# Performance work log

Hardware: AMD Instinct MI355X
Metric: run time of the kernel (lower is better)

Reference implementation:

```python
import jax, jax.numpy as jnp
import numpy as np

N = 50000      # nodes per node type (shared: same edge_index reused across types)
E = 500000     # edges per edge type
H, C = 4, 32   # GATConv heads=4, out_channels = 128 // 4
HID = 128
NEG_SLOPE = 0.2  # PyG GATConv leaky_relu default


def gat(x, src, dst, W, att_src, att_dst, bias):
    """PyG GATConv (eval mode: dropout off), default add_self_loops=True, concat heads."""
    n = x.shape[0]
    xp = (x @ W).reshape(n, H, C)                       # [n, H, C]
    s_src = jnp.einsum('nhc,hc->nh', xp, att_src)       # per-node src scores
    s_dst = jnp.einsum('nhc,hc->nh', xp, att_dst)       # per-node dst scores
    loop = jnp.arange(n, dtype=src.dtype)
    s = jnp.concatenate([src, loop])                    # self-loops appended
    d = jnp.concatenate([dst, loop])
    e = jax.nn.leaky_relu(s_src[s] + s_dst[d], NEG_SLOPE)   # [E+n, H]
    m = jax.ops.segment_max(e, d, num_segments=n)       # segment softmax over incoming edges
    ex = jnp.exp(e - m[d])
    denom = jax.ops.segment_sum(ex, d, num_segments=n)
    alpha = ex / denom[d]                               # [E+n, H]
    out = jax.ops.segment_sum(alpha[:, :, None] * xp[s], d, num_segments=n)  # [n, H, C]
    return out.reshape(n, H * C) + bias


def setup_inputs() -> dict:
    key = jax.random.key(0)
    ks = jax.random.split(key, 24)
    def lin(k, din, dout):
        return (jax.random.normal(k, (din, dout), jnp.float32) / np.sqrt(din)).astype(jnp.float32)
    inp = {}
    inp['x_account'] = jax.random.normal(ks[0], (N, 64), jnp.float32)
    inp['x_customer'] = jax.random.normal(ks[1], (N, 32), jnp.float32)
    inp['x_transaction'] = jax.random.normal(ks[2], (N, 128), jnp.float32)
    inp['ei_transacts'] = jax.random.randint(ks[3], (2, E), 0, N, dtype=jnp.int32)
    inp['ei_owns'] = jax.random.randint(ks[4], (2, E), 0, N, dtype=jnp.int32)
    inp['ei_shares'] = jax.random.randint(ks[5], (2, E), 0, N, dtype=jnp.int32)
    # node embedding Linears
    inp['W_acc'] = lin(ks[6], 64, HID);  inp['b_acc'] = jnp.zeros((HID,), jnp.float32)
    inp['W_cus'] = lin(ks[7], 32, HID);  inp['b_cus'] = jnp.zeros((HID,), jnp.float32)
    inp['W_txn'] = lin(ks[8], 128, HID); inp['b_txn'] = jnp.zeros((HID,), jnp.float32)
    # GATConv params for the two LIVE edge types (first edge type's GATConv is dead code)
    inp['Wg_owns'] = lin(ks[9], HID, H * C)
    inp['as_owns'] = jax.random.normal(ks[10], (H, C), jnp.float32) * 0.1
    inp['ad_owns'] = jax.random.normal(ks[11], (H, C), jnp.float32) * 0.1
    inp['bg_owns'] = jnp.zeros((H * C,), jnp.float32)
    inp['Wg_shares'] = lin(ks[12], HID, H * C)
    inp['as_shares'] = jax.random.normal(ks[13], (H, C), jnp.float32) * 0.1
    inp['ad_shares'] = jax.random.normal(ks[14], (H, C), jnp.float32) * 0.1
    inp['bg_shares'] = jnp.zeros((H * C,), jnp.float32)
    # classifier
    inp['W_cls'] = lin(ks[15], HID, 1); inp['b_cls'] = jnp.zeros((1,), jnp.float32)
    return inp


def reference(x_account, x_customer, x_transaction,
              ei_transacts, ei_owns, ei_shares,
              W_acc, b_acc, W_cus, b_cus, W_txn, b_txn,
              Wg_owns, as_owns, ad_owns, bg_owns,
              Wg_shares, as_shares, ad_shares, bg_shares,
              W_cls, b_cls):
    # per-type embedding (dict insertion order: account, customer, transaction)
    emb = [x_account @ W_acc + b_acc,
           x_customer @ W_cus + b_cus,
           x_transaction @ W_txn + b_txn]
    # edge type 1 ('transacts') initializes final embeddings; types 2,3 add GAT outputs
    finals = []
    for h in emb:
        f = h
        f = f + gat(h, ei_owns[0], ei_owns[1], Wg_owns, as_owns, ad_owns, bg_owns)
        f = f + gat(h, ei_shares[0], ei_shares[1], Wg_shares, as_shares, ad_shares, bg_shares)
        finals.append(f)
    combined = jnp.concatenate(finals, axis=0)          # [3N, HID]
    return jax.nn.sigmoid(combined @ W_cls + b_cls)     # [3N, 1]
```

## Files before the change

kernel.cpp:

```cpp
#include <hip/hip_runtime.h>
#include <hip/hip_bf16.h>
#include <math.h>

#define NNODES 50000
#define NEDGES 500000
#define NTILES 1563

__device__ __forceinline__ float lrelu(float x) { return x > 0.f ? x : 0.2f * x; }

__device__ __forceinline__ unsigned short f2bf(float f) {
    unsigned int u = __float_as_uint(f);
    u += 0x7FFFu + ((u >> 16) & 1u);
    return (unsigned short)(u >> 16);
}

__global__ void wprep_kernel(const float* __restrict__ Wt0, const float* __restrict__ Wt1,
                             const float* __restrict__ Wt2,
                             const float* __restrict__ bt0, const float* __restrict__ bt1,
                             const float* __restrict__ bt2,
                             const float* __restrict__ WgO, const float* __restrict__ WgS,
                             const float* __restrict__ Wc,
                             float* __restrict__ Wcomb, float* __restrict__ wc1,
                             float* __restrict__ bcomb, float* __restrict__ c0) {
    __shared__ float wrow[128];
    const int b = blockIdx.x;
    const int t = threadIdx.x;
    const float* src;
    int isBias = 0, ty = 0, k = 0;
    if (b < 64)       { src = Wt0; k = b;       ty = 0; }
    else if (b < 96)  { src = Wt1; k = b - 64;  ty = 1; }
    else if (b < 224) { src = Wt2; k = b - 96;  ty = 2; }
    else              { isBias = 1; ty = b - 224; src = (ty == 0) ? bt0 : (ty == 1) ? bt1 : bt2; }
    if (t < 128) wrow[t] = isBias ? src[t] : src[k * 128 + t];
    __syncthreads();
    const float* Wg = (t < 128) ? WgO : WgS;
    const int j = t & 127;
    float acc = 0.f;
#pragma unroll 8
    for (int m = 0; m < 128; m++) acc += wrow[m] * Wg[m * 128 + j];
    if (isBias) bcomb[ty * 256 + t] = acc;
    else        Wcomb[b * 256 + t] = acc;
    if (t < 64) {
        float s = wrow[t] * Wc[t] + wrow[t + 64] * Wc[t + 64];
#pragma unroll
        for (int o = 32; o > 0; o >>= 1) s += __shfl_xor(s, o);
        if (t == 0) { if (isBias) c0[ty] = s; else wc1[b] = s; }
    }
}

__launch_bounds__(256)
__global__ void xp_all_b(const float* __restrict__ X0, const float* __restrict__ X1,
                         const float* __restrict__ X2,
                         const float* __restrict__ Wcomb, const float* __restrict__ wc1,
                         const float* __restrict__ bcomb, const float* __restrict__ c0,
                         const float* __restrict__ asO, const float* __restrict__ adO,
                         const float* __restrict__ asS, const float* __restrict__ adS,
                         float* __restrict__ embPart,
                         unsigned short* __restrict__ xpO, unsigned short* __restrict__ xpS,
                         float* __restrict__ ssO, float* __restrict__ sdO,
                         float* __restrict__ ssS, float* __restrict__ sdS, int n) {
    __shared__ float xs[32][128];
    const int t = threadIdx.x;
    const int j4 = t & 31, r = t >> 5;
    const int tile = blockIdx.x % NTILES;
    const int type = blockIdx.x / NTILES;
    const int row0 = tile * 32;

    const float* X;
    int K, ksh, off;
    if (type == 0)      { X = X0; K = 64;  ksh = 4; off = 0;  }
    else if (type == 1) { X = X1; K = 32;  ksh = 3; off = 64; }
    else                { X = X2; K = 128; ksh = 5; off = 96; }
    const size_t tb = (size_t)type * n;

    const int KQ = K >> 2;
    for (int f = t; f < 32 * KQ; f += 256) {
        int row = f >> ksh, kq = f & (KQ - 1);
        float4 v = {0.f, 0.f, 0.f, 0.f};
        if (row0 + row < n) v = *(const float4*)&X[(size_t)(row0 + row) * K + kq * 4];
        *(float4*)&xs[row][kq * 4] = v;
    }
    __syncthreads();

    float4 aO[4], aS[4];
    float dp[4] = {0.f, 0.f, 0.f, 0.f};
#pragma unroll
    for (int p = 0; p < 4; p++) { aO[p] = {0.f, 0.f, 0.f, 0.f}; aS[p] = {0.f, 0.f, 0.f, 0.f}; }
    const float* wb = Wcomb + (size_t)off * 256;
    const float* w1p = wc1 + off;
#pragma unroll 4
    for (int k = 0; k < K; k++) {
        float4 wo = *(const float4*)&wb[k * 256 + j4 * 4];
        float4 ws = *(const float4*)&wb[k * 256 + 128 + j4 * 4];
        float w1 = w1p[k];
        float x0 = xs[r][k], x1 = xs[r + 8][k], x2 = xs[r + 16][k], x3 = xs[r + 24][k];
        aO[0].x += x0 * wo.x; aO[0].y += x0 * wo.y; aO[0].z += x0 * wo.z; aO[0].w += x0 * wo.w;
        aO[1].x += x1 * wo.x; aO[1].y += x1 * wo.y; aO[1].z += x1 * wo.z; aO[1].w += x1 * wo.w;
        aO[2].x += x2 * wo.x; aO[2].y += x2 * wo.y; aO[2].z += x2 * wo.z; aO[2].w += x2 * wo.w;
        aO[3].x += x3 * wo.x; aO[3].y += x3 * wo.y; aO[3].z += x3 * wo.z; aO[3].w += x3 * wo.w;
        aS[0].x += x0 * ws.x; aS[0].y += x0 * ws.y; aS[0].z += x0 * ws.z; aS[0].w += x0 * ws.w;
        aS[1].x += x1 * ws.x; aS[1].y += x1 * ws.y; aS[1].z += x1 * ws.z; aS[1].w += x1 * ws.w;
        aS[2].x += x2 * ws.x; aS[2].y += x2 * ws.y; aS[2].z += x2 * ws.z; aS[2].w += x2 * ws.w;
        aS[3].x += x3 * ws.x; aS[3].y += x3 * ws.y; aS[3].z += x3 * ws.z; aS[3].w += x3 * ws.w;
        dp[0] += x0 * w1; dp[1] += x1 * w1; dp[2] += x2 * w1; dp[3] += x3 * w1;
    }
    float4 bO = *(const float4*)&bcomb[type * 256 + j4 * 4];
    float4 bS = *(const float4*)&bcomb[type * 256 + 128 + j4 * 4];
    const float cc = c0[type];
#pragma unroll
    for (int p = 0; p < 4; p++) {
        aO[p].x += bO.x; aO[p].y += bO.y; aO[p].z += bO.z; aO[p].w += bO.w;
        aS[p].x += bS.x; aS[p].y += bS.y; aS[p].z += bS.z; aS[p].w += bS.w;
    }

    float4 vasO = *(const float4*)&asO[j4 * 4];
    float4 vadO = *(const float4*)&adO[j4 * 4];
    float4 vasS = *(const float4*)&asS[j4 * 4];
    float4 vadS = *(const float4*)&adS[j4 * 4];
#pragma unroll
    for (int p = 0; p < 4; p++) {
        int row = row0 + r + 8 * p;
        if (row < n) {
            ushort4 uo, us;
            uo.x = f2bf(aO[p].x); uo.y = f2bf(aO[p].y); uo.z = f2bf(aO[p].z); uo.w = f2bf(aO[p].w);
            us.x = f2bf(aS[p].x); us.y = f2bf(aS[p].y); us.z = f2bf(aS[p].z); us.w = f2bf(aS[p].w);
            *(ushort4*)&xpO[(tb + row) * 128 + j4 * 4] = uo;
            *(ushort4*)&xpS[(tb + row) * 128 + j4 * 4] = us;
            if (j4 == 0) embPart[tb + row] = dp[p] + cc;
        }
        float psO = aO[p].x * vasO.x + aO[p].y * vasO.y + aO[p].z * vasO.z + aO[p].w * vasO.w;
        float pdO = aO[p].x * vadO.x + aO[p].y * vadO.y + aO[p].z * vadO.z + aO[p].w * vadO.w;
        float psS = aS[p].x * vasS.x + aS[p].y * vasS.y + aS[p].z * vasS.z + aS[p].w * vasS.w;
        float pdS = aS[p].x * vadS.x + aS[p].y * vadS.y + aS[p].z * vadS.z + aS[p].w * vadS.w;
#pragma unroll
        for (int o = 4; o > 0; o >>= 1) {
            psO += __shfl_xor(psO, o);
            pdO += __shfl_xor(pdO, o);
            psS += __shfl_xor(psS, o);
            pdS += __shfl_xor(pdS, o);
        }
        if ((j4 & 7) == 0 && row < n) {
            size_t hidx = (tb + row) * 4 + (j4 >> 3);
            ssO[hidx] = psO; sdO[hidx] = pdO;
            ssS[hidx] = psS; sdS[hidx] = pdS;
        }
    }
}

__global__ void zero_int(int* __restrict__ p, int n) {
    int i = blockIdx.x * blockDim.x + threadIdx.x;
    if (i < n) p[i] = 0;
}

__global__ void count2_kernel(const int* __restrict__ eiO, const int* __restrict__ eiS,
                              int e, int n, int* __restrict__ counts2) {
    int q = blockIdx.x * blockDim.x + threadIdx.x;
    if (q >= 2 * e) return;
    int ty = q >= e;
    int i = ty ? q - e : q;
    const int* ei = ty ? eiS : eiO;
    atomicAdd(&counts2[ty * n + ei[e + i]], 1);
}

__global__ void block_sum_kernel(const int* __restrict__ counts, int n, int* __restrict__ psum) {
    __shared__ int ws[16];
    int tid = threadIdx.x, lane = tid & 63, wid = tid >> 6;
    int i = blockIdx.x * 1024 + tid;
    int v = (i < n) ? counts[i] : 0;
#pragma unroll
    for (int o = 1; o < 64; o <<= 1) v += __shfl_xor(v, o);
    if (lane == 0) ws[wid] = v;
    __syncthreads();
    if (tid < 16) {
        int s = ws[tid];
#pragma unroll
        for (int o = 1; o < 16; o <<= 1) s += __shfl_xor(s, o, 16);
        if (tid == 0) psum[blockIdx.x] = s;
    }
}

__global__ void scan_psum_big(int* __restrict__ psum, int nb, int* __restrict__ total) {
    __shared__ int wsum[2];
    int tid = threadIdx.x, lane = tid & 63, wid = tid >> 6;
    int v = (tid < nb) ? psum[tid] : 0;
    int x = v;
#pragma unroll
    for (int o = 1; o < 64; o <<= 1) {
        int t = __shfl_up(x, o);
        if (lane >= o) x += t;
    }
    if (lane == 63) wsum[wid] = x;
    __syncthreads();
    int base = (wid == 1) ? wsum[0] : 0;
    if (tid < nb) psum[tid] = base + x - v;
    if (tid == 127) *total = wsum[0] + wsum[1];
}

__global__ void scan_block_kernel(const int* __restrict__ counts, const int* __restrict__ psum,
                                  int n, int* __restrict__ row_ptr, int* __restrict__ cursor) {
    __shared__ int ws[16];
    int tid = threadIdx.x, lane = tid & 63, wid = tid >> 6;
    int i = blockIdx.x * 1024 + tid;
    int v = (i < n) ? counts[i] : 0;
    int x = v;
#pragma unroll
    for (int o = 1; o < 64; o <<= 1) {
        int t = __shfl_up(x, o);
        if (lane >= o) x += t;
    }
    if (lane == 63) ws[wid] = x;
    __syncthreads();
    if (tid < 16) {
        int s = ws[tid];
#pragma unroll
        for (int o = 1; o < 16; o <<= 1) {
            int t = __shfl_up(s, o, 16);
            if (tid >= o) s += t;
        }
        ws[tid] = s;
    }
    __syncthreads();
    int base = psum[blockIdx.x] + (wid ? ws[wid - 1] : 0);
    int excl = base + x - v;
    if (i < n) { row_ptr[i] = excl; cursor[i] = excl; }
}

__global__ void scatter2_kernel(const int* __restrict__ eiO, const int* __restrict__ eiS,
                                int e, int n, int* __restrict__ cursor2,
                                long long* __restrict__ cp2) {
    int q = blockIdx.x * blockDim.x + threadIdx.x;
    if (q >= 2 * e) return;
    int ty = q >= e;
    int i = ty ? q - e : q;
    const int* ei = ty ? eiS : eiO;
    int d = ei[e + i];
    int p = atomicAdd(&cursor2[ty * n + d], 1);
    cp2[p] = ((long long)i << 32) | (unsigned)ei[i];
}

__global__ void sort_rows_kernel(const int* __restrict__ rp, long long* __restrict__ cp, int n) {
    int i = blockIdx.x * blockDim.x + threadIdx.x;
    if (i >= n) return;
    int r0 = rp[i], r1 = rp[i + 1];
    for (int a = r0 + 1; a < r1; a++) {
        long long v = cp[a];
        int b = a - 1;
        while (b >= r0 && cp[b] > v) {
            cp[b + 1] = cp[b];
            b--;
        }
        cp[b + 1] = v;
    }
}

__global__ void alpha6_kernel(const int* __restrict__ eiO, const int* __restrict__ eiS,
                              const float* __restrict__ ssO, const float* __restrict__ sdO,
                              const float* __restrict__ ssS, const float* __restrict__ sdS,
                              float* __restrict__ alO, float* __restrict__ alS, int e, int n) {
    int q = blockIdx.x * blockDim.x + threadIdx.x;
    if (q >= 6 * e) return;
    int ty = q / (2 * e);
    int rem = q - ty * 2 * e;
    const size_t nb = (size_t)ty * n * 4;
    const size_t eb = (size_t)ty * e * 4;
    const int* ei;
    const float* ss;
    const float* sd;
    float* al;
    int i;
    if (rem < e) { ei = eiO; ss = ssO + nb; sd = sdO + nb; al = alO + eb; i = rem; }
    else         { ei = eiS; ss = ssS + nb; sd = sdS + nb; al = alS + eb; i = rem - e; }
    int s = ei[i], d = ei[e + i];
    float4 svs = *(const float4*)&ss[s * 4];
    float4 svd = *(const float4*)&ss[d * 4];
    float4 dvd = *(const float4*)&sd[d * 4];
    float4 a;
    a.x = __expf(lrelu(svs.x + dvd.x) - lrelu(svd.x + dvd.x));
    a.y = __expf(lrelu(svs.y + dvd.y) - lrelu(svd.y + dvd.y));
    a.z = __expf(lrelu(svs.z + dvd.z) - lrelu(svd.z + dvd.z));
    a.w = __expf(lrelu(svs.w + dvd.w) - lrelu(svd.w + dvd.w));
    *(float4*)&al[(size_t)i * 4] = a;
}

__global__ void gat_fused_b(const unsigned short* __restrict__ xpO, const float* __restrict__ alO,
                            const unsigned short* __restrict__ xpS, const float* __restrict__ alS,
                            const long long* __restrict__ cp2, const int* __restrict__ rp2,
                            const float* __restrict__ bgO, const float* __restrict__ bgS,
                            const float* __restrict__ embPart, const float* __restrict__ Wc,
                            const float* __restrict__ bc, float* __restrict__ out, int n) {
    const int wave = threadIdx.x >> 6, lane = threadIdx.x & 63;
    const int i3 = blockIdx.x * 4 + wave;
    if (i3 >= 3 * n) return;
    const int ty = i3 / n, i = i3 - ty * n;
    const int c = lane * 2, hh = lane >> 4;

    const unsigned short* xo = xpO + (size_t)ty * n * 128;
    const unsigned short* xs_ = xpS + (size_t)ty * n * 128;
    const float* alo = alO + (size_t)ty * NEDGES * 4;
    const float* als = alS + (size_t)ty * NEDGES * 4;

    const int r0o = rp2[i], r1o = rp2[i + 1];
    const int r0s = rp2[n + i], r1s = rp2[n + i + 1];

    float tO = 0.f, oxO = 0.f, oyO = 0.f;
    float tS = 0.f, oxS = 0.f, oyS = 0.f;
    int ko = r0o, ks = r0s;

    while (ko + 2 <= r1o && ks + 2 <= r1s) {
        long long vo0 = cp2[ko], vo1 = cp2[ko + 1];
        long long vs0 = cp2[ks], vs1 = cp2[ks + 1];
        int so0 = (int)(vo0 & 0xFFFFFFFFll), eo0 = (int)(vo0 >> 32);
        int so1 = (int)(vo1 & 0xFFFFFFFFll), eo1 = (int)(vo1 >> 32);
        int sx0 = (int)(vs0 & 0xFFFFFFFFll), es0 = (int)(vs0 >> 32);
        int sx1 = (int)(vs1 & 0xFFFFFFFFll), es1 = (int)(vs1 >> 32);
        float ao0 = alo[(size_t)eo0 * 4 + hh], ao1 = alo[(size_t)eo1 * 4 + hh];
        float as0 = als[(size_t)es0 * 4 + hh], as1 = als[(size_t)es1 * 4 + hh];
        unsigned uo0 = *(const unsigned*)&xo[(size_t)so0 * 128 + c];
        unsigned uo1 = *(const unsigned*)&xo[(size_t)so1 * 128 + c];
        unsigned us0 = *(const unsigned*)&xs_[(size_t)sx0 * 128 + c];
        unsigned us1 = *(const unsigned*)&xs_[(size_t)sx1 * 128 + c];
        tO += ao0 + ao1;
        oxO += ao0 * __uint_as_float(uo0 << 16) + ao1 * __uint_as_float(uo1 << 16);
        oyO += ao0 * __uint_as_float(uo0 & 0xFFFF0000u) + ao1 * __uint_as_float(uo1 & 0xFFFF0000u);
        tS += as0 + as1;
        oxS += as0 * __uint_as_float(us0 << 16) + as1 * __uint_as_float(us1 << 16);
        oyS += as0 * __uint_as_float(us0 & 0xFFFF0000u) + as1 * __uint_as_float(us1 & 0xFFFF0000u);
        ko += 2; ks += 2;
    }
    while (ko < r1o && ks < r1s) {
        long long vo = cp2[ko], vs = cp2[ks];
        int so = (int)(vo & 0xFFFFFFFFll), eo = (int)(vo >> 32);
        int sx = (int)(vs & 0xFFFFFFFFll), es = (int)(vs >> 32);
        float ao = alo[(size_t)eo * 4 + hh];
        float as_ = als[(size_t)es * 4 + hh];
        unsigned uo = *(const unsigned*)&xo[(size_t)so * 128 + c];
        unsigned us = *(const unsigned*)&xs_[(size_t)sx * 128 + c];
        tO += ao;
        oxO += ao * __uint_as_float(uo << 16);
        oyO += ao * __uint_as_float(uo & 0xFFFF0000u);
        tS += as_;
        oxS += as_ * __uint_as_float(us << 16);
        oyS += as_ * __uint_as_float(us & 0xFFFF0000u);
        ko++; ks++;
    }
    for (; ko + 2 <= r1o; ko += 2) {
        long long vo0 = cp2[ko], vo1 = cp2[ko + 1];
        int so0 = (int)(vo0 & 0xFFFFFFFFll), eo0 = (int)(vo0 >> 32);
        int so1 = (int)(vo1 & 0xFFFFFFFFll), eo1 = (int)(vo1 >> 32);
        float ao0 = alo[(size_t)eo0 * 4 + hh], ao1 = alo[(size_t)eo1 * 4 + hh];
        unsigned uo0 = *(const unsigned*)&xo[(size_t)so0 * 128 + c];
        unsigned uo1 = *(const unsigned*)&xo[(size_t)so1 * 128 + c];
        tO += ao0 + ao1;
        oxO += ao0 * __uint_as_float(uo0 << 16) + ao1 * __uint_as_float(uo1 << 16);
        oyO += ao0 * __uint_as_float(uo0 & 0xFFFF0000u) + ao1 * __uint_as_float(uo1 & 0xFFFF0000u);
    }
    for (; ko < r1o; ko++) {
        long long vo = cp2[ko];
        int so = (int)(vo & 0xFFFFFFFFll), eo = (int)(vo >> 32);
        float ao = alo[(size_t)eo * 4 + hh];
        unsigned uo = *(const unsigned*)&xo[(size_t)so * 128 + c];
        tO += ao;
        oxO += ao * __uint_as_float(uo << 16);
        oyO += ao * __uint_as_float(uo & 0xFFFF0000u);
    }
    for (; ks + 2 <= r1s; ks += 2) {
        long long vs0 = cp2[ks], vs1 = cp2[ks + 1];
        int sx0 = (int)(vs0 & 0xFFFFFFFFll), es0 = (int)(vs0 >> 32);
        int sx1 = (int)(vs1 & 0xFFFFFFFFll), es1 = (int)(vs1 >> 32);
        float as0 = als[(size_t)es0 * 4 + hh], as1 = als[(size_t)es1 * 4 + hh];
        unsigned us0 = *(const unsigned*)&xs_[(size_t)sx0 * 128 + c];
        unsigned us1 = *(const unsigned*)&xs_[(size_t)sx1 * 128 + c];
        tS += as0 + as1;
        oxS += as0 * __uint_as_float(us0 << 16) + as1 * __uint_as_float(us1 << 16);
        oyS += as0 * __uint_as_float(us0 & 0xFFFF0000u) + as1 * __uint_as_float(us1 & 0xFFFF0000u);
    }
    for (; ks < r1s; ks++) {
        long long vs = cp2[ks];
        int sx = (int)(vs & 0xFFFFFFFFll), es = (int)(vs >> 32);
        float as_ = als[(size_t)es * 4 + hh];
        unsigned us = *(const unsigned*)&xs_[(size_t)sx * 128 + c];
        tS += as_;
        oxS += as_ * __uint_as_float(us << 16);
        oyS += as_ * __uint_as_float(us & 0xFFFF0000u);
    }
    {
        unsigned uo = *(const unsigned*)&xo[(size_t)i * 128 + c];
        unsigned us = *(const unsigned*)&xs_[(size_t)i * 128 + c];
        oxO += __uint_as_float(uo << 16);
        oyO += __uint_as_float(uo & 0xFFFF0000u);
        oxS += __uint_as_float(us << 16);
        oyS += __uint_as_float(us & 0xFFFF0000u);
    }
    const float idO = 1.f / (tO + 1.f), idS = 1.f / (tS + 1.f);
    float fx = idO * oxO + idS * oxS + bgO[c] + bgS[c];
    float fy = idO * oyO + idS * oyS + bgO[c + 1] + bgS[c + 1];

    float2 w = *(const float2*)&Wc[c];
    float p = fx * w.x + fy * w.y;
#pragma unroll
    for (int o = 32; o > 0; o >>= 1) p += __shfl_xor(p, o);
    if (lane == 0) out[i3] = 1.f / (1.f + expf(-(p + embPart[i3] + bc[0])));
}

extern "C" void kernel_launch(void* const* d_in, const int* in_sizes, int n_in,
                              void* d_out, int out_size, void* d_ws, size_t ws_size,
                              hipStream_t stream) {
    const int N = NNODES, E = NEDGES;
    const float* x_acc = (const float*)d_in[0];
    const float* x_cus = (const float*)d_in[1];
    const float* x_txn = (const float*)d_in[2];
    const int* ei_owns = (const int*)d_in[4];
    const int* ei_shr = (const int*)d_in[5];
    const float* W_acc = (const float*)d_in[6];
    const float* b_acc = (const float*)d_in[7];
    const float* W_cus = (const float*)d_in[8];
    const float* b_cus = (const float*)d_in[9];
    const float* W_txn = (const float*)d_in[10];
    const float* b_txn = (const float*)d_in[11];
    const float* Wg_o = (const float*)d_in[12];
    const float* as_o = (const float*)d_in[13];
    const float* ad_o = (const float*)d_in[14];
    const float* bg_o = (const float*)d_in[15];
    const float* Wg_s = (const float*)d_in[16];
    const float* as_s = (const float*)d_in[17];
    const float* ad_s = (const float*)d_in[18];
    const float* bg_s = (const float*)d_in[19];
    const float* W_cls = (const float*)d_in[20];
    const float* b_cls = (const float*)d_in[21];
    float* out = (float*)d_out;

    float* wf = (float*)d_ws;
    int* iw = (int*)d_ws;
    unsigned short* xp_o3 = (unsigned short*)(wf + 0);
    unsigned short* xp_s3 = (unsigned short*)(wf + 9600000);
    float* ss_o3 = wf + 19200000;
    float* sd_o3 = wf + 19800000;
    float* ss_s3 = wf + 20400000;
    float* sd_s3 = wf + 21000000;
    float* al_o3 = wf + 21600000;
    float* al_s3 = wf + 27600000;
    float* embPart = wf + 33600000;
    int* rp2    = iw + 33750008;
    long long* cp2 = (long long*)(iw + 33850016);
    float* Wcomb = wf + 35850016;
    float* wc1   = wf + 35907360;
    float* bcomb = wf + 35907584;
    float* c0    = wf + 35908352;
    int* counts2 = (int*)al_o3;
    int* cursor2 = counts2 + 100000;
    int* psum    = cursor2 + 100000;

    const int gN2 = (2 * N + 255) / 256;
    const int gE2 = (2 * E + 255) / 256;
    const int gS2 = (2 * N + 1023) / 1024;
    const int gXP = 3 * NTILES;
    const int gA = (3 * N + 3) / 4;
    const int gA6 = (6 * E + 255) / 256;

    wprep_kernel<<<227, 256, 0, stream>>>(W_acc, W_cus, W_txn, b_acc, b_cus, b_txn,
                                          Wg_o, Wg_s, W_cls, Wcomb, wc1, bcomb, c0);

    zero_int<<<gN2, 256, 0, stream>>>(counts2, 2 * N);
    count2_kernel<<<gE2, 256, 0, stream>>>(ei_owns, ei_shr, E, N, counts2);
    block_sum_kernel<<<gS2, 1024, 0, stream>>>(counts2, 2 * N, psum);
    scan_psum_big<<<1, 128, 0, stream>>>(psum, gS2, rp2 + 2 * N);
    scan_block_kernel<<<gS2, 1024, 0, stream>>>(counts2, psum, 2 * N, rp2, cursor2);
    scatter2_kernel<<<gE2, 256, 0, stream>>>(ei_owns, ei_shr, E, N, cursor2, cp2);
    sort_rows_kernel<<<gN2, 256, 0, stream>>>(rp2, cp2, 2 * N);

    xp_all_b<<<gXP, 256, 0, stream>>>(x_acc, x_cus, x_txn,
                                      Wcomb, wc1, bcomb, c0,
                                      as_o, ad_o, as_s, ad_s,
                                      embPart, xp_o3, xp_s3,
                                      ss_o3, sd_o3, ss_s3, sd_s3, N);
    alpha6_kernel<<<gA6, 256, 0, stream>>>(ei_owns, ei_shr,
                                           ss_o3, sd_o3, ss_s3, sd_s3,
                                           al_o3, al_s3, E, N);
    gat_fused_b<<<gA, 256, 0, stream>>>(xp_o3, al_o3, xp_s3, al_s3,
                                        cp2, rp2, bg_o, bg_s,
                                        embPart, W_cls, b_cls, out, N);
}
```

Measured before the change: 505.4 us.

## Store attention coefficients in CSR slot order to make aggregation reads contiguous

The alpha kernel now walks the sorted CSR edge array instead of the original edge order. For each slot it computes coefficients for all three node types and writes them at the slot position. The aggregation kernel can then read alpha sequentially by slot index rather than gathering by edge id, which turns a random 4-float gather per edge into streaming reads. The cost is that the alpha kernel now gathers the destination index and scores in CSR order, and it can only start after the sort has finished.

```diff
diff --git a/kernel.cpp b/kernel.cpp
--- a/kernel.cpp
+++ b/kernel.cpp
@@ -253,37 +253,38 @@
     }
 }
 
-__global__ void alpha6_kernel(const int* __restrict__ eiO, const int* __restrict__ eiS,
-                              const float* __restrict__ ssO, const float* __restrict__ sdO,
-                              const float* __restrict__ ssS, const float* __restrict__ sdS,
-                              float* __restrict__ alO, float* __restrict__ alS, int e, int n) {
+__global__ void alpha_slot_kernel(const int* __restrict__ eiO, const int* __restrict__ eiS,
+                                  const long long* __restrict__ cp2,
+                                  const float* __restrict__ ssO, const float* __restrict__ sdO,
+                                  const float* __restrict__ ssS, const float* __restrict__ sdS,
+                                  float* __restrict__ al3, int e, int n) {
     int q = blockIdx.x * blockDim.x + threadIdx.x;
-    if (q >= 6 * e) return;
-    int ty = q / (2 * e);
-    int rem = q - ty * 2 * e;
-    const size_t nb = (size_t)ty * n * 4;
-    const size_t eb = (size_t)ty * e * 4;
-    const int* ei;
-    const float* ss;
-    const float* sd;
-    float* al;
-    int i;
-    if (rem < e) { ei = eiO; ss = ssO + nb; sd = sdO + nb; al = alO + eb; i = rem; }
-    else         { ei = eiS; ss = ssS + nb; sd = sdS + nb; al = alS + eb; i = rem - e; }
-    int s = ei[i], d = ei[e + i];
-    float4 svs = *(const float4*)&ss[s * 4];
-    float4 svd = *(const float4*)&ss[d * 4];
-    float4 dvd = *(const float4*)&sd[d * 4];
-    float4 a;
-    a.x = __expf(lrelu(svs.x + dvd.x) - lrelu(svd.x + dvd.x));
-    a.y = __expf(lrelu(svs.y + dvd.y) - lrelu(svd.y + dvd.y));
-    a.z = __expf(lrelu(svs.z + dvd.z) - lrelu(svd.z + dvd.z));
-    a.w = __expf(lrelu(svs.w + dvd.w) - lrelu(svd.w + dvd.w));
-    *(float4*)&al[(size_t)i * 4] = a;
-}
-
-__global__ void gat_fused_b(const unsigned short* __restrict__ xpO, const float* __restrict__ alO,
-                            const unsigned short* __restrict__ xpS, const float* __restrict__ alS,
+    if (q >= 2 * e) return;
+    long long v = cp2[q];
+    int s = (int)(v & 0xFFFFFFFFll), eid = (int)(v >> 32);
+    int conv = q >= e;
+    int d = (conv ? eiS : eiO)[e + eid];
+    const float* ssb = conv ? ssS : ssO;
+    const float* sdb = conv ? sdS : sdO;
+#pragma unroll
+    for (int ty = 0; ty < 3; ty++) {
+        const float* ss = ssb + (size_t)ty * n * 4;
+        const float* sd = sdb + (size_t)ty * n * 4;
+        float4 svs = *(const float4*)&ss[s * 4];
+        float4 svd = *(const float4*)&ss[d * 4];
+        float4 dvd = *(const float4*)&sd[d * 4];
+        float4 a;
+        a.x = __expf(lrelu(svs.x + dvd.x) - lrelu(svd.x + dvd.x));
+        a.y = __expf(lrelu(svs.y + dvd.y) - lrelu(svd.y + dvd.y));
+        a.z = __expf(lrelu(svs.z + dvd.z) - lrelu(svd.z + dvd.z));
+        a.w = __expf(lrelu(svs.w + dvd.w) - lrelu(svd.w + dvd.w));
+        *(float4*)&al3[((size_t)ty * 2 * e + q) * 4] = a;
+    }
+}
+
+__global__ void gat_fused_b(const unsigned short* __restrict__ xpO,
+                            const unsigned short* __restrict__ xpS,
+                            const float* __restrict__ al3,
                             const long long* __restrict__ cp2, const int* __restrict__ rp2,
                             const float* __restrict__ bgO, const float* __restrict__ bgS,
                             const float* __restrict__ embPart, const float* __restrict__ Wc,
@@ -296,8 +297,7 @@
 
     const unsigned short* xo = xpO + (size_t)ty * n * 128;
     const unsigned short* xs_ = xpS + (size_t)ty * n * 128;
-    const float* alo = alO + (size_t)ty * NEDGES * 4;
-    const float* als = alS + (size_t)ty * NEDGES * 4;
+    const float* alB = al3 + (size_t)ty * 2 * NEDGES * 4;
 
     const int r0o = rp2[i], r1o = rp2[i + 1];
     const int r0s = rp2[n + i], r1s = rp2[n + i + 1];
@@ -309,12 +309,10 @@
     while (ko + 2 <= r1o && ks + 2 <= r1s) {
         long long vo0 = cp2[ko], vo1 = cp2[ko + 1];
         long long vs0 = cp2[ks], vs1 = cp2[ks + 1];
-        int so0 = (int)(vo0 & 0xFFFFFFFFll), eo0 = (int)(vo0 >> 32);
-        int so1 = (int)(vo1 & 0xFFFFFFFFll), eo1 = (int)(vo1 >> 32);
-        int sx0 = (int)(vs0 & 0xFFFFFFFFll), es0 = (int)(vs0 >> 32);
-        int sx1 = (int)(vs1 & 0xFFFFFFFFll), es1 = (int)(vs1 >> 32);
-        float ao0 = alo[(size_t)eo0 * 4 + hh], ao1 = alo[(size_t)eo1 * 4 + hh];
-        float as0 = als[(size_t)es0 * 4 + hh], as1 = als[(size_t)es1 * 4 + hh];
+        int so0 = (int)(vo0 & 0xFFFFFFFFll), so1 = (int)(vo1 & 0xFFFFFFFFll);
+        int sx0 = (int)(vs0 & 0xFFFFFFFFll), sx1 = (int)(vs1 & 0xFFFFFFFFll);
+        float ao0 = alB[(size_t)ko * 4 + hh], ao1 = alB[(size_t)(ko + 1) * 4 + hh];
+        float as0 = alB[(size_t)ks * 4 + hh], as1 = alB[(size_t)(ks + 1) * 4 + hh];
         unsigned uo0 = *(const unsigned*)&xo[(size_t)so0 * 128 + c];
         unsigned uo1 = *(const unsigned*)&xo[(size_t)so1 * 128 + c];
         unsigned us0 = *(const unsigned*)&xs_[(size_t)sx0 * 128 + c];
@@ -329,10 +327,9 @@
     }
     while (ko < r1o && ks < r1s) {
         long long vo = cp2[ko], vs = cp2[ks];
-        int so = (int)(vo & 0xFFFFFFFFll), eo = (int)(vo >> 32);
-        int sx = (int)(vs & 0xFFFFFFFFll), es = (int)(vs >> 32);
-        float ao = alo[(size_t)eo * 4 + hh];
-        float as_ = als[(size_t)es * 4 + hh];
+        int so = (int)(vo & 0xFFFFFFFFll), sx = (int)(vs & 0xFFFFFFFFll);
+        float ao = alB[(size_t)ko * 4 + hh];
+        float as_ = alB[(size_t)ks * 4 + hh];
         unsigned uo = *(const unsigned*)&xo[(size_t)so * 128 + c];
         unsigned us = *(const unsigned*)&xs_[(size_t)sx * 128 + c];
         tO += ao;
@@ -345,9 +342,8 @@
     }
     for (; ko + 2 <= r1o; ko += 2) {
         long long vo0 = cp2[ko], vo1 = cp2[ko + 1];
-        int so0 = (int)(vo0 & 0xFFFFFFFFll), eo0 = (int)(vo0 >> 32);
-        int so1 = (int)(vo1 & 0xFFFFFFFFll), eo1 = (int)(vo1 >> 32);
-        float ao0 = alo[(size_t)eo0 * 4 + hh], ao1 = alo[(size_t)eo1 * 4 + hh];
+        int so0 = (int)(vo0 & 0xFFFFFFFFll), so1 = (int)(vo1 & 0xFFFFFFFFll);
+        float ao0 = alB[(size_t)ko * 4 + hh], ao1 = alB[(size_t)(ko + 1) * 4 + hh];
         unsigned uo0 = *(const unsigned*)&xo[(size_t)so0 * 128 + c];
         unsigned uo1 = *(const unsigned*)&xo[(size_t)so1 * 128 + c];
         tO += ao0 + ao1;
@@ -356,8 +352,8 @@
     }
     for (; ko < r1o; ko++) {
         long long vo = cp2[ko];
-        int so = (int)(vo & 0xFFFFFFFFll), eo = (int)(vo >> 32);
-        float ao = alo[(size_t)eo * 4 + hh];
+        int so = (int)(vo & 0xFFFFFFFFll);
+        float ao = alB[(size_t)ko * 4 + hh];
         unsigned uo = *(const unsigned*)&xo[(size_t)so * 128 + c];
         tO += ao;
         oxO += ao * __uint_as_float(uo << 16);
@@ -365,9 +361,8 @@
     }
     for (; ks + 2 <= r1s; ks += 2) {
         long long vs0 = cp2[ks], vs1 = cp2[ks + 1];
-        int sx0 = (int)(vs0 & 0xFFFFFFFFll), es0 = (int)(vs0 >> 32);
-        int sx1 = (int)(vs1 & 0xFFFFFFFFll), es1 = (int)(vs1 >> 32);
-        float as0 = als[(size_t)es0 * 4 + hh], as1 = als[(size_t)es1 * 4 + hh];
+        int sx0 = (int)(vs0 & 0xFFFFFFFFll), sx1 = (int)(vs1 & 0xFFFFFFFFll);
+        float as0 = alB[(size_t)ks * 4 + hh], as1 = alB[(size_t)(ks + 1) * 4 + hh];
         unsigned us0 = *(const unsigned*)&xs_[(size_t)sx0 * 128 + c];
         unsigned us1 = *(const unsigned*)&xs_[(size_t)sx1 * 128 + c];
         tS += as0 + as1;
@@ -376,8 +371,8 @@
     }
     for (; ks < r1s; ks++) {
         long long vs = cp2[ks];
-        int sx = (int)(vs & 0xFFFFFFFFll), es = (int)(vs >> 32);
-        float as_ = als[(size_t)es * 4 + hh];
+        int sx = (int)(vs & 0xFFFFFFFFll);
+        float as_ = alB[(size_t)ks * 4 + hh];
         unsigned us = *(const unsigned*)&xs_[(size_t)sx * 128 + c];
         tS += as_;
         oxS += as_ * __uint_as_float(us << 16);
@@ -437,8 +432,7 @@
     float* sd_o3 = wf + 19800000;
     float* ss_s3 = wf + 20400000;
     float* sd_s3 = wf + 21000000;
-    float* al_o3 = wf + 21600000;
-    float* al_s3 = wf + 27600000;
+    float* al3   = wf + 21600000;
     float* embPart = wf + 33600000;
     int* rp2    = iw + 33750008;
     long long* cp2 = (long long*)(iw + 33850016);
@@ -446,7 +440,7 @@
     float* wc1   = wf + 35907360;
     float* bcomb = wf + 35907584;
     float* c0    = wf + 35908352;
-    int* counts2 = (int*)al_o3;
+    int* counts2 = (int*)al3;
     int* cursor2 = counts2 + 100000;
     int* psum    = cursor2 + 100000;
 
@@ -455,7 +449,6 @@
     const int gS2 = (2 * N + 1023) / 1024;
     const int gXP = 3 * NTILES;
     const int gA = (3 * N + 3) / 4;
-    const int gA6 = (6 * E + 255) / 256;
 
     wprep_kernel<<<227, 256, 0, stream>>>(W_acc, W_cus, W_txn, b_acc, b_cus, b_txn,
                                           Wg_o, Wg_s, W_cls, Wcomb, wc1, bcomb, c0);
@@ -473,10 +466,10 @@
                                       as_o, ad_o, as_s, ad_s,
                                       embPart, xp_o3, xp_s3,
                                       ss_o3, sd_o3, ss_s3, sd_s3, N);
-    alpha6_kernel<<<gA6, 256, 0, stream>>>(ei_owns, ei_shr,
-                                           ss_o3, sd_o3, ss_s3, sd_s3,
-                                           al_o3, al_s3, E, N);
-    gat_fused_b<<<gA, 256, 0, stream>>>(xp_o3, al_o3, xp_s3, al_s3,
+    alpha_slot_kernel<<<gE2, 256, 0, stream>>>(ei_owns, ei_shr, cp2,
+                                               ss_o3, sd_o3, ss_s3, sd_s3,
+                                               al3, E, N);
+    gat_fused_b<<<gA, 256, 0, stream>>>(xp_o3, xp_s3, al3,
                                         cp2, rp2, bg_o, bg_s,
                                         embPart, W_cls, b_cls, out, N);
 }
```

Result: faster. 466.4 us, median of 2 (-7.7%).
